# Kernel tuning notes

Hardware: AMD Instinct MI355X
Metric: run time of the kernel (lower is better)

## Reference

```python
import jax, jax.numpy as jnp
import numpy as np

N = 27            # hardcoded node count in the module
D = 1024          # state_dim
E = D * 5         # MHA embed dim = 5120
H = 4             # n_heads


def setup_inputs() -> dict:
    key = jax.random.key(0)
    ks = jax.random.split(key, 6)
    s = 0.02
    return {
        "node_states": jax.random.normal(ks[0], (N, D, 5), jnp.float32),
        "hist_prev": jax.random.normal(ks[1], (N, D, 5), jnp.float32),
        "granger_w": jax.random.normal(ks[2], (1, 2 * E), jnp.float32) * s,
        "granger_b": jnp.zeros((1,), jnp.float32),
        "in_proj_w": jax.random.normal(ks[3], (3 * E, E), jnp.float32) * s,
        "in_proj_b": jnp.zeros((3 * E,), jnp.float32),
        "out_proj_w": jax.random.normal(ks[4], (E, E), jnp.float32) * s,
        "out_proj_b": jnp.zeros((E,), jnp.float32),
        "light_hertz": 500,
    }


def _mha(x, in_w, in_b, out_w, out_b):
    # x: [N, E]; torch MultiheadAttention with q=k=v=x, batch of 1
    qkv = x @ in_w.T + in_b                       # [N, 3E]
    q, k, v = jnp.split(qkv, 3, axis=-1)          # each [N, E]
    hd = E // H
    q = q.reshape(N, H, hd).transpose(1, 0, 2)    # [H, N, hd]
    k = k.reshape(N, H, hd).transpose(1, 0, 2)
    v = v.reshape(N, H, hd).transpose(1, 0, 2)
    scores = jnp.einsum('hqd,hkd->hqk', q, k) / jnp.sqrt(jnp.float32(hd))
    attn = jax.nn.softmax(scores, axis=-1)        # [H, N, N]
    o = jnp.einsum('hqk,hkd->hqd', attn, v)       # [H, N, hd]
    o = o.transpose(1, 0, 2).reshape(N, E)
    return o @ out_w.T + out_b                    # [N, E]


def reference(node_states, hist_prev, granger_w, granger_b,
              in_proj_w, in_proj_b, out_proj_w, out_proj_b, light_hertz):
    node_flat = node_states.reshape(N, E)         # [N, E]
    hist_flat = hist_prev.reshape(N, E)           # [N, E]

    # Granger pairwise test, vectorized: pred_input = [hist[j], node[i]]
    # score[i, j] = sigmoid(hist[j] . w_h + node[i] . w_n + b)
    w_h = granger_w[0, :E]
    w_n = granger_w[0, E:]
    col = node_flat @ w_n                          # [N] -> varies with i
    row = hist_flat @ w_h                          # [N] -> varies with j
    adj = jax.nn.sigmoid(col[:, None] + row[None, :] + granger_b[0])  # [N, N]
    causal_adj = adj * (1.0 - jnp.eye(N, dtype=adj.dtype))            # zero diagonal

    hertz_weight = jnp.clip(jnp.float32(light_hertz) / 1000.0, 0.1, 1.0)
    attended = _mha(node_flat, in_proj_w, in_proj_b, out_proj_w, out_proj_b)
    out = (attended * hertz_weight).reshape(N, D, 5)
    return out, causal_adj
```

## Files before the change

### kernel.cpp

```cpp
#include <hip/hip_runtime.h>

#define NROW 27
#define EDIM 5120
#define QKVDIM 15360
#define HD 1280

typedef __attribute__((ext_vector_type(8))) short bf16x8;
typedef __attribute__((ext_vector_type(4))) float f32x4;

__device__ inline short f2bf(float x) {
    unsigned u = __builtin_bit_cast(unsigned, x);
    u = (u + 0x7FFFu + ((u >> 16) & 1u)) >> 16;
    return (short)u;
}
__device__ inline float bf2f(short h) {
    unsigned u = ((unsigned)(unsigned short)h) << 16;
    return __builtin_bit_cast(float, u);
}

#define KC 64
#define LDK 72

__device__ inline void loadW8(float* wbuf, const float* wp) {
    #pragma unroll
    for (int i = 0; i < 8; ++i)
        *(float4*)&wbuf[4 * i] = ((const float4*)wp)[i];
}
__device__ inline void loadX2(float* xbuf, const float* xp, bool xok) {
    if (xok) {
        *(float4*)&xbuf[0] = ((const float4*)xp)[0];
        *(float4*)&xbuf[4] = ((const float4*)xp)[1];
    } else {
        #pragma unroll
        for (int j = 0; j < 8; ++j) xbuf[j] = 0.f;
    }
}

__global__ __launch_bounds__(256)
void gemm_bf16x2(const float* __restrict__ X, const float* __restrict__ W,
                 float* __restrict__ Cp, int K, int Ntot, int Kblk)
{
    __shared__ short Whi[128][LDK];
    __shared__ short Wlo[128][LDK];
    __shared__ short Xhi[32][LDK];
    __shared__ short Xlo[32][LDK];

    const int tid = threadIdx.x;
    const int n0 = blockIdx.x * 128;
    const int k0 = blockIdx.y * Kblk;

    const int lane = tid & 63;
    const int wv   = tid >> 6;
    const int lm   = lane & 15;
    const int q8   = (lane >> 4) * 8;

    f32x4 acc[2][2] = {};

    const int wr  = tid >> 1;
    const int wkh = (tid & 1) * 32;
    const float* wp = W + (size_t)(n0 + wr) * K + k0 + wkh;
    const int xr = tid >> 3;
    const int xk = (tid & 7) * 8;
    const bool xok = (xr < NROW);
    const float* xp = X + (size_t)(xok ? xr : 0) * K + k0 + xk;

    float wbuf[32], xbuf[8];
    loadW8(wbuf, wp);
    loadX2(xbuf, xp, xok);

    for (int kc = 0; kc < Kblk; kc += KC) {
        #pragma unroll
        for (int g = 0; g < 4; ++g) {
            bf16x8 h8, l8;
            #pragma unroll
            for (int j = 0; j < 8; ++j) {
                float f = wbuf[8 * g + j];
                short h = f2bf(f);
                h8[j] = h;
                l8[j] = f2bf(f - bf2f(h));
            }
            *(bf16x8*)&Whi[wr][wkh + 8 * g] = h8;
            *(bf16x8*)&Wlo[wr][wkh + 8 * g] = l8;
        }
        {
            bf16x8 h8, l8;
            #pragma unroll
            for (int j = 0; j < 8; ++j) {
                short h = f2bf(xbuf[j]);
                h8[j] = h;
                l8[j] = f2bf(xbuf[j] - bf2f(h));
            }
            *(bf16x8*)&Xhi[xr][xk] = h8;
            *(bf16x8*)&Xlo[xr][xk] = l8;
        }
        __syncthreads();

        if (kc + KC < Kblk) {
            wp += KC; xp += KC;
            loadW8(wbuf, wp);
            loadX2(xbuf, xp, xok);
        }

        #pragma unroll
        for (int s = 0; s < 2; ++s) {
            const int ko = 32 * s + q8;
            bf16x8 ah0 = *(const bf16x8*)&Xhi[lm][ko];
            bf16x8 ah1 = *(const bf16x8*)&Xhi[lm + 16][ko];
            bf16x8 al0 = *(const bf16x8*)&Xlo[lm][ko];
            bf16x8 al1 = *(const bf16x8*)&Xlo[lm + 16][ko];
            bf16x8 bh0 = *(const bf16x8*)&Whi[32 * wv + lm][ko];
            bf16x8 bh1 = *(const bf16x8*)&Whi[32 * wv + 16 + lm][ko];
            bf16x8 bl0 = *(const bf16x8*)&Wlo[32 * wv + lm][ko];
            bf16x8 bl1 = *(const bf16x8*)&Wlo[32 * wv + 16 + lm][ko];

            acc[0][0] = __builtin_amdgcn_mfma_f32_16x16x32_bf16(ah0, bh0, acc[0][0], 0, 0, 0);
            acc[0][0] = __builtin_amdgcn_mfma_f32_16x16x32_bf16(ah0, bl0, acc[0][0], 0, 0, 0);
            acc[0][0] = __builtin_amdgcn_mfma_f32_16x16x32_bf16(al0, bh0, acc[0][0], 0, 0, 0);

            acc[0][1] = __builtin_amdgcn_mfma_f32_16x16x32_bf16(ah0, bh1, acc[0][1], 0, 0, 0);
            acc[0][1] = __builtin_amdgcn_mfma_f32_16x16x32_bf16(ah0, bl1, acc[0][1], 0, 0, 0);
            acc[0][1] = __builtin_amdgcn_mfma_f32_16x16x32_bf16(al0, bh1, acc[0][1], 0, 0, 0);

            acc[1][0] = __builtin_amdgcn_mfma_f32_16x16x32_bf16(ah1, bh0, acc[1][0], 0, 0, 0);
            acc[1][0] = __builtin_amdgcn_mfma_f32_16x16x32_bf16(ah1, bl0, acc[1][0], 0, 0, 0);
            acc[1][0] = __builtin_amdgcn_mfma_f32_16x16x32_bf16(al1, bh0, acc[1][0], 0, 0, 0);

            acc[1][1] = __builtin_amdgcn_mfma_f32_16x16x32_bf16(ah1, bh1, acc[1][1], 0, 0, 0);
            acc[1][1] = __builtin_amdgcn_mfma_f32_16x16x32_bf16(ah1, bl1, acc[1][1], 0, 0, 0);
            acc[1][1] = __builtin_amdgcn_mfma_f32_16x16x32_bf16(al1, bh1, acc[1][1], 0, 0, 0);
        }
        __syncthreads();
    }

    const size_t base = (size_t)blockIdx.y * NROW * Ntot;
    #pragma unroll
    for (int mi = 0; mi < 2; ++mi) {
        #pragma unroll
        for (int r = 0; r < 4; ++r) {
            const int m = mi * 16 + (lane >> 4) * 4 + r;
            if (m < NROW) {
                #pragma unroll
                for (int ni = 0; ni < 2; ++ni) {
                    const int n = n0 + 32 * wv + ni * 16 + lm;
                    Cp[base + (size_t)m * Ntot + n] = acc[mi][ni][r];
                }
            }
        }
    }
}

__global__ __launch_bounds__(256)
void reduce_kernel(const float* __restrict__ Cp, const float* __restrict__ bias,
                   float* __restrict__ out, int Ntot, int nky, const int* __restrict__ hz,
                   const float* __restrict__ cr, const float* __restrict__ gb,
                   float* __restrict__ adj)
{
    if (adj && blockIdx.x == gridDim.x - 1) {
        for (int t = threadIdx.x; t < NROW * NROW; t += 256) {
            const int i = t / NROW, j = t % NROW;
            float v = 0.f;
            if (i != j) {
                float z = cr[i] + cr[NROW + j] + gb[0];
                v = 1.0f / (1.0f + expf(-z));
            }
            adj[t] = v;
        }
        return;
    }
    const int idx = blockIdx.x * 256 + threadIdx.x;
    const int total4 = NROW * Ntot / 4;
    if (idx >= total4) return;
    float4 s = ((const float4*)Cp)[idx];
    for (int k = 1; k < nky; ++k) {
        float4 p = ((const float4*)(Cp + (size_t)k * NROW * Ntot))[idx];
        s.x += p.x; s.y += p.y; s.z += p.z; s.w += p.w;
    }
    const int n = (idx * 4) % Ntot;
    float4 b = *(const float4*)(bias + n);
    s.x += b.x; s.y += b.y; s.z += b.z; s.w += b.w;
    if (hz) {
        float h = (float)hz[0] * 0.001f;
        float sc = fminf(fmaxf(h, 0.1f), 1.0f);
        s.x *= sc; s.y *= sc; s.z *= sc; s.w *= sc;
    }
    ((float4*)out)[idx] = s;
}

__global__ __launch_bounds__(256)
void colrow_kernel(const float* __restrict__ node, const float* __restrict__ hist,
                   const float* __restrict__ gw, float* __restrict__ cr)
{
    const int b = blockIdx.x;
    const float* x = (b < NROW) ? node + (size_t)b * EDIM : hist + (size_t)(b - NROW) * EDIM;
    const float* w = (b < NROW) ? gw + EDIM : gw;
    const int tid = threadIdx.x;
    float a = 0.f;
    for (int f = tid; f < EDIM / 4; f += 256) {
        float4 xv = ((const float4*)x)[f];
        float4 wv = ((const float4*)w)[f];
        a += xv.x * wv.x + xv.y * wv.y + xv.z * wv.z + xv.w * wv.w;
    }
    #pragma unroll
    for (int off = 32; off; off >>= 1) a += __shfl_down(a, off);
    __shared__ float red[4];
    if ((tid & 63) == 0) red[tid >> 6] = a;
    __syncthreads();
    if (tid == 0) cr[b] = red[0] + red[1] + red[2] + red[3];
}

__global__ __launch_bounds__(256)
void attn_kernel(const float* __restrict__ qkv, float* __restrict__ O)
{
    __shared__ float qs[HD];
    __shared__ float sc[NROW];
    __shared__ float pr[NROW];
    const int bx = blockIdx.x;
    const int h = bx & 3;
    const int i = bx >> 2;
    const int tid = threadIdx.x;

    const size_t qoff = (size_t)i * QKVDIM + (size_t)h * HD;
    for (int d = tid; d < HD; d += 256) qs[d] = qkv[qoff + d];
    __syncthreads();

    const int wid = tid >> 6, lane = tid & 63;
    for (int j = wid; j < NROW; j += 4) {
        const float* kr = qkv + (size_t)j * QKVDIM + EDIM + (size_t)h * HD;
        float a = 0.f;
        #pragma unroll
        for (int it = 0; it < 5; ++it) {
            int d4 = lane + 64 * it;
            float4 k4 = *(const float4*)(kr + 4 * d4);
            float4 q4 = *(const float4*)(qs + 4 * d4);
            a += q4.x * k4.x + q4.y * k4.y + q4.z * k4.z + q4.w * k4.w;
        }
        #pragma unroll
        for (int off = 32; off; off >>= 1) a += __shfl_down(a, off);
        if (lane == 0) sc[j] = a * 0.02795084971874737f;
    }
    __syncthreads();

    float mxv = -1e30f;
    for (int j = 0; j < NROW; ++j) mxv = fmaxf(mxv, sc[j]);
    float s = 0.f;
    for (int j = 0; j < NROW; ++j) s += expf(sc[j] - mxv);
    if (tid < NROW) pr[tid] = expf(sc[tid] - mxv) / s;
    __syncthreads();

    for (int d4 = tid; d4 < HD / 4; d4 += 256) {
        float4 o = make_float4(0.f, 0.f, 0.f, 0.f);
        for (int j = 0; j < NROW; ++j) {
            const float4 v4 = *(const float4*)(qkv + (size_t)j * QKVDIM + 2 * EDIM + (size_t)h * HD + 4 * d4);
            const float p = pr[j];
            o.x = fmaf(p, v4.x, o.x);
            o.y = fmaf(p, v4.y, o.y);
            o.z = fmaf(p, v4.z, o.z);
            o.w = fmaf(p, v4.w, o.w);
        }
        *(float4*)(O + (size_t)i * EDIM + (size_t)h * HD + 4 * d4) = o;
    }
}

extern "C" void kernel_launch(void* const* d_in, const int* in_sizes, int n_in,
                              void* d_out, int out_size, void* d_ws, size_t ws_size,
                              hipStream_t stream)
{
    const float* node = (const float*)d_in[0];
    const float* hist = (const float*)d_in[1];
    const float* gw   = (const float*)d_in[2];
    const float* gb   = (const float*)d_in[3];
    const float* inw  = (const float*)d_in[4];
    const float* inb  = (const float*)d_in[5];
    const float* outw = (const float*)d_in[6];
    const float* outb = (const float*)d_in[7];
    const int*   hz   = (const int*)d_in[8];

    float* out = (float*)d_out;

    float* Cp1  = (float*)d_ws;
    float* qkvf = Cp1 + (size_t)8 * NROW * QKVDIM;
    float* Obuf = qkvf + (size_t)NROW * QKVDIM;
    float* Cp2  = Obuf + (size_t)NROW * EDIM;
    float* cr   = Cp2 + (size_t)16 * NROW * EDIM;

    colrow_kernel<<<54, 256, 0, stream>>>(node, hist, gw, cr);

    gemm_bf16x2<<<dim3(120, 8), 256, 0, stream>>>(node, inw, Cp1, EDIM, QKVDIM, EDIM / 8);
    reduce_kernel<<<NROW * QKVDIM / 4 / 256, 256, 0, stream>>>(
        Cp1, inb, qkvf, QKVDIM, 8, nullptr, nullptr, nullptr, nullptr);

    attn_kernel<<<108, 256, 0, stream>>>(qkvf, Obuf);

    gemm_bf16x2<<<dim3(40, 16), 256, 0, stream>>>(Obuf, outw, Cp2, EDIM, EDIM, EDIM / 16);
    reduce_kernel<<<NROW * EDIM / 4 / 256 + 1, 256, 0, stream>>>(
        Cp2, outb, out, EDIM, 16, hz, cr, gb, out + (size_t)NROW * EDIM);
}
```

Before: 540.1 us.

## Load weights via global_load_lds and pre-split activations to bf16 hi/lo

Weight tiles now go straight from global memory into LDS as fp32 through global_load_lds, and are split into bf16 hi/lo in registers at MFMA time. The old path staged them through registers, converted them, then wrote to LDS. Activations are pre-split into hi/lo bf16 arrays by a new convert kernel, or directly in the attention epilogue, and read from global memory or cache inside the GEMM. This cuts register staging and LDS conversion work on the bandwidth-bound weight stream. The cost is losing the register prefetch overlap, since loads are now issued and then synced with no double buffering. The LDS layout Wf[128][64] has no padding, so the MFMA fragment reads may hit bank conflicts.

```diff
diff --git a/kernel.cpp b/kernel.cpp
--- a/kernel.cpp
+++ b/kernel.cpp
@@ -8,42 +8,36 @@
 typedef __attribute__((ext_vector_type(8))) short bf16x8;
 typedef __attribute__((ext_vector_type(4))) float f32x4;
 
-__device__ inline short f2bf(float x) {
+__device__ __forceinline__ short f2bf(float x) {
     unsigned u = __builtin_bit_cast(unsigned, x);
     u = (u + 0x7FFFu + ((u >> 16) & 1u)) >> 16;
     return (short)u;
 }
-__device__ inline float bf2f(short h) {
+__device__ __forceinline__ float bf2f(short h) {
     unsigned u = ((unsigned)(unsigned short)h) << 16;
     return __builtin_bit_cast(float, u);
 }
 
+__device__ __forceinline__ void cvt8(const float* w, bf16x8& hi, bf16x8& lo) {
+    float4 a = *(const float4*)w;
+    float4 b = *(const float4*)(w + 4);
+    float f[8] = {a.x, a.y, a.z, a.w, b.x, b.y, b.z, b.w};
+    #pragma unroll
+    for (int j = 0; j < 8; ++j) {
+        short h = f2bf(f[j]);
+        hi[j] = h;
+        lo[j] = f2bf(f[j] - bf2f(h));
+    }
+}
+
 #define KC 64
-#define LDK 72
-
-__device__ inline void loadW8(float* wbuf, const float* wp) {
-    #pragma unroll
-    for (int i = 0; i < 8; ++i)
-        *(float4*)&wbuf[4 * i] = ((const float4*)wp)[i];
-}
-__device__ inline void loadX2(float* xbuf, const float* xp, bool xok) {
-    if (xok) {
-        *(float4*)&xbuf[0] = ((const float4*)xp)[0];
-        *(float4*)&xbuf[4] = ((const float4*)xp)[1];
-    } else {
-        #pragma unroll
-        for (int j = 0; j < 8; ++j) xbuf[j] = 0.f;
-    }
-}
-
-__global__ __launch_bounds__(256)
-void gemm_bf16x2(const float* __restrict__ X, const float* __restrict__ W,
-                 float* __restrict__ Cp, int K, int Ntot, int Kblk)
-{
-    __shared__ short Whi[128][LDK];
-    __shared__ short Wlo[128][LDK];
-    __shared__ short Xhi[32][LDK];
-    __shared__ short Xlo[32][LDK];
+
+__global__ __launch_bounds__(256)
+void gemm_glds(const short* __restrict__ Xhi, const short* __restrict__ Xlo,
+               const float* __restrict__ W, float* __restrict__ Cp,
+               int K, int Ntot, int Kblk)
+{
+    __shared__ float Wf[128][KC];
 
     const int tid = threadIdx.x;
     const int n0 = blockIdx.x * 128;
@@ -53,65 +47,38 @@
     const int wv   = tid >> 6;
     const int lm   = lane & 15;
     const int q8   = (lane >> 4) * 8;
+    const int rA1  = (lm + 16 < NROW) ? lm + 16 : 0;
 
     f32x4 acc[2][2] = {};
 
-    const int wr  = tid >> 1;
-    const int wkh = (tid & 1) * 32;
-    const float* wp = W + (size_t)(n0 + wr) * K + k0 + wkh;
-    const int xr = tid >> 3;
-    const int xk = (tid & 7) * 8;
-    const bool xok = (xr < NROW);
-    const float* xp = X + (size_t)(xok ? xr : 0) * K + k0 + xk;
-
-    float wbuf[32], xbuf[8];
-    loadW8(wbuf, wp);
-    loadX2(xbuf, xp, xok);
+    const float* wp = W + (size_t)(n0 + (tid >> 4)) * K + k0 + 4 * (tid & 15);
+    char* lds0 = (char*)&Wf[0][0] + tid * 16;
+
+    const short* pAh0 = Xhi + (size_t)lm  * K + k0;
+    const short* pAh1 = Xhi + (size_t)rA1 * K + k0;
+    const short* pAl0 = Xlo + (size_t)lm  * K + k0;
+    const short* pAl1 = Xlo + (size_t)rA1 * K + k0;
 
     for (int kc = 0; kc < Kblk; kc += KC) {
         #pragma unroll
-        for (int g = 0; g < 4; ++g) {
-            bf16x8 h8, l8;
-            #pragma unroll
-            for (int j = 0; j < 8; ++j) {
-                float f = wbuf[8 * g + j];
-                short h = f2bf(f);
-                h8[j] = h;
-                l8[j] = f2bf(f - bf2f(h));
-            }
-            *(bf16x8*)&Whi[wr][wkh + 8 * g] = h8;
-            *(bf16x8*)&Wlo[wr][wkh + 8 * g] = l8;
-        }
-        {
-            bf16x8 h8, l8;
-            #pragma unroll
-            for (int j = 0; j < 8; ++j) {
-                short h = f2bf(xbuf[j]);
-                h8[j] = h;
-                l8[j] = f2bf(xbuf[j] - bf2f(h));
-            }
-            *(bf16x8*)&Xhi[xr][xk] = h8;
-            *(bf16x8*)&Xlo[xr][xk] = l8;
-        }
+        for (int i = 0; i < 8; ++i)
+            __builtin_amdgcn_global_load_lds(
+                (const __attribute__((address_space(1))) unsigned*)(wp + (size_t)i * 16 * K),
+                (__attribute__((address_space(3))) unsigned*)(lds0 + i * 4096),
+                16, 0, 0);
         __syncthreads();
-
-        if (kc + KC < Kblk) {
-            wp += KC; xp += KC;
-            loadW8(wbuf, wp);
-            loadX2(xbuf, xp, xok);
-        }
 
         #pragma unroll
         for (int s = 0; s < 2; ++s) {
             const int ko = 32 * s + q8;
-            bf16x8 ah0 = *(const bf16x8*)&Xhi[lm][ko];
-            bf16x8 ah1 = *(const bf16x8*)&Xhi[lm + 16][ko];
-            bf16x8 al0 = *(const bf16x8*)&Xlo[lm][ko];
-            bf16x8 al1 = *(const bf16x8*)&Xlo[lm + 16][ko];
-            bf16x8 bh0 = *(const bf16x8*)&Whi[32 * wv + lm][ko];
-            bf16x8 bh1 = *(const bf16x8*)&Whi[32 * wv + 16 + lm][ko];
-            bf16x8 bl0 = *(const bf16x8*)&Wlo[32 * wv + lm][ko];
-            bf16x8 bl1 = *(const bf16x8*)&Wlo[32 * wv + 16 + lm][ko];
+            bf16x8 ah0 = *(const bf16x8*)(pAh0 + ko);
+            bf16x8 ah1 = *(const bf16x8*)(pAh1 + ko);
+            bf16x8 al0 = *(const bf16x8*)(pAl0 + ko);
+            bf16x8 al1 = *(const bf16x8*)(pAl1 + ko);
+
+            bf16x8 bh0, bl0, bh1, bl1;
+            cvt8(&Wf[32 * wv + lm][ko],      bh0, bl0);
+            cvt8(&Wf[32 * wv + 16 + lm][ko], bh1, bl1);
 
             acc[0][0] = __builtin_amdgcn_mfma_f32_16x16x32_bf16(ah0, bh0, acc[0][0], 0, 0, 0);
             acc[0][0] = __builtin_amdgcn_mfma_f32_16x16x32_bf16(ah0, bl0, acc[0][0], 0, 0, 0);
@@ -130,6 +97,9 @@
             acc[1][1] = __builtin_amdgcn_mfma_f32_16x16x32_bf16(al1, bh1, acc[1][1], 0, 0, 0);
         }
         __syncthreads();
+
+        wp += KC;
+        pAh0 += KC; pAh1 += KC; pAl0 += KC; pAl1 += KC;
     }
 
     const size_t base = (size_t)blockIdx.y * NROW * Ntot;
@@ -150,6 +120,28 @@
 }
 
 __global__ __launch_bounds__(256)
+void convert_bf(const float* __restrict__ x, short* __restrict__ hi,
+                short* __restrict__ lo, int n4)
+{
+    const int idx = blockIdx.x * 256 + threadIdx.x;
+    if (idx >= n4) return;
+    float4 v = ((const float4*)x)[idx];
+    float f[4] = {v.x, v.y, v.z, v.w};
+    short4 h, l;
+    short hh[4], ll[4];
+    #pragma unroll
+    for (int j = 0; j < 4; ++j) {
+        short t = f2bf(f[j]);
+        hh[j] = t;
+        ll[j] = f2bf(f[j] - bf2f(t));
+    }
+    h.x = hh[0]; h.y = hh[1]; h.z = hh[2]; h.w = hh[3];
+    l.x = ll[0]; l.y = ll[1]; l.z = ll[2]; l.w = ll[3];
+    ((short4*)hi)[idx] = h;
+    ((short4*)lo)[idx] = l;
+}
+
+__global__ __launch_bounds__(256)
 void reduce_kernel(const float* __restrict__ Cp, const float* __restrict__ bias,
                    float* __restrict__ out, int Ntot, int nky, const int* __restrict__ hz,
                    const float* __restrict__ cr, const float* __restrict__ gb,
@@ -209,7 +201,8 @@
 }
 
 __global__ __launch_bounds__(256)
-void attn_kernel(const float* __restrict__ qkv, float* __restrict__ O)
+void attn_kernel(const float* __restrict__ qkv, short* __restrict__ Ohi,
+                 short* __restrict__ Olo)
 {
     __shared__ float qs[HD];
     __shared__ float sc[NROW];
@@ -257,7 +250,20 @@
             o.z = fmaf(p, v4.z, o.z);
             o.w = fmaf(p, v4.w, o.w);
         }
-        *(float4*)(O + (size_t)i * EDIM + (size_t)h * HD + 4 * d4) = o;
+        float f[4] = {o.x, o.y, o.z, o.w};
+        short4 hv, lv;
+        short hh[4], ll[4];
+        #pragma unroll
+        for (int j = 0; j < 4; ++j) {
+            short t = f2bf(f[j]);
+            hh[j] = t;
+            ll[j] = f2bf(f[j] - bf2f(t));
+        }
+        hv.x = hh[0]; hv.y = hh[1]; hv.z = hh[2]; hv.w = hh[3];
+        lv.x = ll[0]; lv.y = ll[1]; lv.z = ll[2]; lv.w = ll[3];
+        const size_t oidx = ((size_t)i * EDIM + (size_t)h * HD + 4 * d4) / 4;
+        ((short4*)Ohi)[oidx] = hv;
+        ((short4*)Olo)[oidx] = lv;
     }
 }
 
@@ -279,19 +285,23 @@
 
     float* Cp1  = (float*)d_ws;
     float* qkvf = Cp1 + (size_t)8 * NROW * QKVDIM;
-    float* Obuf = qkvf + (size_t)NROW * QKVDIM;
-    float* Cp2  = Obuf + (size_t)NROW * EDIM;
+    float* Cp2  = qkvf + (size_t)NROW * QKVDIM;
     float* cr   = Cp2 + (size_t)16 * NROW * EDIM;
+    short* Xhi  = (short*)(cr + 64);
+    short* Xlo  = Xhi + (size_t)NROW * EDIM;
+    short* Ohi  = Xlo + (size_t)NROW * EDIM;
+    short* Olo  = Ohi + (size_t)NROW * EDIM;
 
     colrow_kernel<<<54, 256, 0, stream>>>(node, hist, gw, cr);
-
-    gemm_bf16x2<<<dim3(120, 8), 256, 0, stream>>>(node, inw, Cp1, EDIM, QKVDIM, EDIM / 8);
+    convert_bf<<<NROW * EDIM / 4 / 256, 256, 0, stream>>>(node, Xhi, Xlo, NROW * EDIM / 4);
+
+    gemm_glds<<<dim3(120, 8), 256, 0, stream>>>(Xhi, Xlo, inw, Cp1, EDIM, QKVDIM, EDIM / 8);
     reduce_kernel<<<NROW * QKVDIM / 4 / 256, 256, 0, stream>>>(
         Cp1, inb, qkvf, QKVDIM, 8, nullptr, nullptr, nullptr, nullptr);
 
-    attn_kernel<<<108, 256, 0, stream>>>(qkvf, Obuf);
-
-    gemm_bf16x2<<<dim3(40, 16), 256, 0, stream>>>(Obuf, outw, Cp2, EDIM, EDIM, EDIM / 16);
+    attn_kernel<<<108, 256, 0, stream>>>(qkvf, Ohi, Olo);
+
+    gemm_glds<<<dim3(40, 16), 256, 0, stream>>>(Ohi, Olo, outw, Cp2, EDIM, EDIM, EDIM / 16);
     reduce_kernel<<<NROW * EDIM / 4 / 256 + 1, 256, 0, stream>>>(
         Cp2, outb, out, EDIM, 16, hz, cr, gb, out + (size_t)NROW * EDIM);
 }
```

After: 541.1 us. No clear change (+0.2%).
